# Optimization experiments

Measured on AMD Instinct MI355X. Metric: run time of the kernel, lower is better.

## Reference

```python
import math
import jax, jax.numpy as jnp
import numpy as np

HEADS = 16
REL_WINDOW = 128


def setup_inputs() -> dict:
    key = jax.random.key(0)
    k1, k2, k3, k4, k5 = jax.random.split(key, 5)
    b, s, d = 2, 2048, 1024
    hd = d // HEADS          # 64
    R = 2 * REL_WINDOW + 1   # 257
    return {
        "x": jax.random.normal(k1, (b, s, d), dtype=jnp.float32),
        "Wqkv": jax.random.normal(k2, (3 * d, d), dtype=jnp.float32) * (1.0 / math.sqrt(d)),
        "bqkv": jax.random.normal(k3, (3 * d,), dtype=jnp.float32) * 0.02,
        "Wr": jax.random.normal(k4, (R, hd), dtype=jnp.float32) * (1.0 / math.sqrt(hd)),
        "br": jax.random.normal(k5, (R,), dtype=jnp.float32) * 0.02,
    }


def reference(x, Wqkv, bqkv, Wr, br):
    b, s, d = x.shape
    h = HEADS
    hd = d // h
    w = REL_WINDOW
    scale = math.sqrt(d / h)

    # qkv projection; torch view(b,s,h,3*hd) then chunk(3, dim=-1)
    qkv = (x @ Wqkv.T + bqkv).reshape(b, s, h, 3 * hd)
    q, k, v = jnp.split(qkv, 3, axis=-1)          # each [b,s,h,hd]
    q = q.transpose(0, 2, 1, 3)                   # [b,h,s,hd]
    k = k.transpose(0, 2, 1, 3)
    v = v.transpose(0, 2, 1, 3)

    # content scores
    content = jnp.einsum('bhik,bhjk->bhij', q, k) / scale  # [b,h,s,s]

    # relative position scores: project queries to R logits, gather per (i,j) offset
    idx = jnp.arange(s)
    offsets = jnp.clip(idx[None, :] - idx[:, None], -w, w) + w  # [s,s] in [0, 2w]
    rp = jnp.einsum('bhik,rk->bhir', q, Wr) + br               # [b,h,s,R]
    pos = jnp.take_along_axis(rp, jnp.broadcast_to(offsets, (b, h, s, s)), axis=-1)

    attn = jax.nn.softmax(content + pos, axis=-1)
    out = jnp.einsum('bhij,bhjk->bhik', attn, v)  # [b,h,s,hd]
    return out.transpose(0, 2, 1, 3).reshape(b, s, d)
```

## Files before the change

### kernel.cpp

```cpp
#include <hip/hip_runtime.h>

typedef short bfrag __attribute__((ext_vector_type(8)));
typedef float f32x4 __attribute__((ext_vector_type(4)));

#define MFMA16(a, b, c) __builtin_amdgcn_mfma_f32_16x16x32_bf16((a), (b), (c), 0, 0, 0)

#define SEQ   2048
#define DMOD  1024
#define NHEAD 16
#define HDIM  64
#define RSZ   257
#define RSTRIDE 260
#define RPADN 272
#define XN    (4096*1024)
#define WN    (3072*1024)
#define LOG2E 1.44269504f

__device__ __forceinline__ unsigned short f2bf(float f) {
  unsigned int u = __float_as_uint(f);
  u += 0x7FFFu + ((u >> 16) & 1u);
  return (unsigned short)(u >> 16);
}
__device__ __forceinline__ float bf2f(unsigned short u) {
  return __uint_as_float(((unsigned int)u) << 16);
}
__device__ __forceinline__ unsigned int pkbf(float a, float b) {
#if defined(__gfx950__)
  unsigned int r;
  asm("v_cvt_pk_bf16_f32 %0, %1, %2" : "=v"(r) : "v"(a), "v"(b));
  return r;
#else
  return (unsigned int)f2bf(a) | ((unsigned int)f2bf(b) << 16);
#endif
}
__device__ __forceinline__ float fexp2(float x) {
#if __has_builtin(__builtin_amdgcn_exp2f)
  return __builtin_amdgcn_exp2f(x);
#else
  return __expf(x * 0.69314718f);
#endif
}
__device__ __forceinline__ void gl2lds16(const void* g, void* l) {
  __builtin_amdgcn_global_load_lds(
      (__attribute__((address_space(1))) void*)(g),
      (__attribute__((address_space(3))) void*)(l), 16, 0, 0);
}

__global__ __launch_bounds__(256) void cast_all(const float* __restrict__ x,
                                                const float* __restrict__ Wqkv,
                                                const float* __restrict__ Wr,
                                                unsigned short* __restrict__ xb,
                                                unsigned short* __restrict__ wb,
                                                unsigned short* __restrict__ wrb) {
  int i = (blockIdx.x * 256 + threadIdx.x) * 4;
  if (i < XN) {
    float4 v = *(const float4*)(x + i);
    ushort4 o; o.x = f2bf(v.x); o.y = f2bf(v.y); o.z = f2bf(v.z); o.w = f2bf(v.w);
    *(ushort4*)(xb + i) = o;
  } else if (i < XN + WN) {
    int j = i - XN;
    float4 v = *(const float4*)(Wqkv + j);
    ushort4 o; o.x = f2bf(v.x); o.y = f2bf(v.y); o.z = f2bf(v.z); o.w = f2bf(v.w);
    *(ushort4*)(wb + j) = o;
  } else {
    int j = i - XN - WN;
    ushort4 o;
    unsigned short t[4];
#pragma unroll
    for (int k = 0; k < 4; ++k)
      t[k] = (j + k < RSZ * HDIM) ? f2bf(Wr[j + k]) : (unsigned short)0;
    o.x = t[0]; o.y = t[1]; o.z = t[2]; o.w = t[3];
    *(ushort4*)(wrb + j) = o;
  }
}

__global__ __launch_bounds__(256) void qkv_gemm(const unsigned short* __restrict__ xb,
                                                const unsigned short* __restrict__ wb,
                                                const float* __restrict__ bqkv,
                                                unsigned short* __restrict__ qb,
                                                unsigned short* __restrict__ kbuf,
                                                unsigned short* __restrict__ vtb) {
  __shared__ unsigned short SMEM[2 * 128 * 64];
  unsigned short* As = SMEM;
  unsigned short* Bs = SMEM + 128 * 64;
  unsigned short* Vtmp = SMEM;
  const int tid = threadIdx.x;
  const int m0 = blockIdx.y * 128, n0 = blockIdx.x * 128;
  const int wave = tid >> 6, lane = tid & 63;
  const int q4 = lane >> 4, l16 = lane & 15;
  const int wm = (wave & 1) * 64, wn = (wave >> 1) * 64;
  const int sw = l16 & 7;

  f32x4 acc[4][4];
#pragma unroll
  for (int rt = 0; rt < 4; ++rt)
#pragma unroll
    for (int ct = 0; ct < 4; ++ct) acc[rt][ct] = (f32x4){0.f, 0.f, 0.f, 0.f};

  for (int k0 = 0; k0 < DMOD; k0 += 64) {
#pragma unroll
    for (int it = 0; it < 4; ++it) {
      int ch = it * 256 + tid;
      int r = ch >> 3, cl = (ch & 7) ^ (r & 7);
      gl2lds16(xb + (size_t)(m0 + r) * DMOD + k0 + cl * 8, As + ch * 8);
      gl2lds16(wb + (size_t)(n0 + r) * DMOD + k0 + cl * 8, Bs + ch * 8);
    }
    __syncthreads();
#pragma unroll
    for (int ks = 0; ks < 2; ++ks) {
      bfrag af[4], bf[4];
#pragma unroll
      for (int rt = 0; rt < 4; ++rt)
        af[rt] = *(const bfrag*)(As + (wm + rt * 16 + l16) * 64 + ((ks * 4 + q4) ^ sw) * 8);
#pragma unroll
      for (int ct = 0; ct < 4; ++ct)
        bf[ct] = *(const bfrag*)(Bs + (wn + ct * 16 + l16) * 64 + ((ks * 4 + q4) ^ sw) * 8);
#pragma unroll
      for (int rt = 0; rt < 4; ++rt)
#pragma unroll
        for (int ct = 0; ct < 4; ++ct)
          acc[rt][ct] = MFMA16(bf[ct], af[rt], acc[rt][ct]);
    }
    __syncthreads();
  }

  const int batch = m0 >> 11;
  const int sbase = m0 & 2047;
  const int r3 = blockIdx.x % 3;
  const bool hasV = (r3 != 0);
  const int nv0 = n0 + ((r3 == 2) ? 64 : 0);

#pragma unroll
  for (int ct = 0; ct < 4; ++ct) {
    int ng = n0 + wn + ct * 16 + q4 * 4;
    int hh = ng / 192;
    int rem = ng - hh * 192;
    int t = rem >> 6, dd = rem & 63;
    float4 b4 = *(const float4*)(bqkv + ng);
    if (t < 2) {
      unsigned short* dst = (t == 0) ? qb : kbuf;
      size_t rowo = ((size_t)(batch * NHEAD + hh)) * SEQ + sbase;
#pragma unroll
      for (int rt = 0; rt < 4; ++rt) {
        int m = wm + rt * 16 + l16;
        uint2 pv;
        pv.x = pkbf(acc[rt][ct][0] + b4.x, acc[rt][ct][1] + b4.y);
        pv.y = pkbf(acc[rt][ct][2] + b4.z, acc[rt][ct][3] + b4.w);
        *(uint2*)(dst + (rowo + m) * HDIM + dd) = pv;
      }
    } else {
#pragma unroll
      for (int rt = 0; rt < 4; ++rt) {
        int m = wm + rt * 16 + l16;
        Vtmp[(dd + 0) * 136 + m] = f2bf(acc[rt][ct][0] + b4.x);
        Vtmp[(dd + 1) * 136 + m] = f2bf(acc[rt][ct][1] + b4.y);
        Vtmp[(dd + 2) * 136 + m] = f2bf(acc[rt][ct][2] + b4.z);
        Vtmp[(dd + 3) * 136 + m] = f2bf(acc[rt][ct][3] + b4.w);
      }
    }
  }

  if (hasV) {
    __syncthreads();
    const int hh = nv0 / 192;
    unsigned short* vdst = vtb + ((size_t)(batch * NHEAD + hh)) * HDIM * SEQ;
#pragma unroll
    for (int it = 0; it < 4; ++it) {
      int u = it * 256 + tid;
      int dd = u >> 4, mc = u & 15;
      bfrag val = *(const bfrag*)(Vtmp + dd * 136 + mc * 8);
      *(bfrag*)(vdst + (size_t)dd * SEQ + sbase + mc * 8) = val;
    }
  }
}

__global__ __launch_bounds__(256) void rp_gemm(const unsigned short* __restrict__ qb,
                                               const unsigned short* __restrict__ wrb,
                                               const float* __restrict__ br,
                                               unsigned short* __restrict__ rp16) {
  __shared__ unsigned short WrS[RPADN * HDIM];
  __shared__ unsigned short Qs[64 * HDIM];
  const int tid = threadIdx.x;
  const size_t row0 = (size_t)blockIdx.x * 64;

  for (int i = tid; i < RPADN * HDIM / 8; i += 256)
    *(uint4*)(&WrS[i * 8]) = *(const uint4*)(&wrb[i * 8]);
  for (int i = tid; i < 512; i += 256)
    *(uint4*)(&Qs[i * 8]) = *(const uint4*)(&qb[row0 * HDIM + i * 8]);
  __syncthreads();

  const int wave = tid >> 6, lane = tid & 63;
  const int q4 = lane >> 4, l16 = lane & 15;

  bfrag af0 = *(const bfrag*)(Qs + (wave * 16 + l16) * 64 + q4 * 8);
  bfrag af1 = *(const bfrag*)(Qs + (wave * 16 + l16) * 64 + 32 + q4 * 8);

  unsigned short* rrow = rp16 + (row0 + wave * 16 + l16) * RSTRIDE;
  const float br256 = br[256];

#pragma unroll 4
  for (int ct = 0; ct < 16; ++ct) {
    f32x4 acc = (f32x4){0.f, 0.f, 0.f, 0.f};
    bfrag w0 = *(const bfrag*)(WrS + (ct * 16 + l16) * 64 + q4 * 8);
    bfrag w1 = *(const bfrag*)(WrS + (ct * 16 + l16) * 64 + 32 + q4 * 8);
    acc = MFMA16(w0, af0, acc);
    acc = MFMA16(w1, af1, acc);
    int r = ct * 16 + q4 * 4;
    float4 b4 = *(const float4*)(br + r);
    uint2 pv;
    pv.x = pkbf((acc[0] + b4.x) * LOG2E, (acc[1] + b4.y) * LOG2E);
    pv.y = pkbf((acc[2] + b4.z) * LOG2E, (acc[3] + b4.w) * LOG2E);
    *(uint2*)(rrow + r) = pv;
  }
  {
    f32x4 acc = (f32x4){0.f, 0.f, 0.f, 0.f};
    bfrag w0 = *(const bfrag*)(WrS + (256 + l16) * 64 + q4 * 8);
    bfrag w1 = *(const bfrag*)(WrS + (256 + l16) * 64 + 32 + q4 * 8);
    acc = MFMA16(w0, af0, acc);
    acc = MFMA16(w1, af1, acc);
    if (q4 == 0)
      rrow[256] = f2bf((acc[0] + br256) * LOG2E);
  }
}

__global__ __launch_bounds__(512) void flash_attn(const unsigned short* __restrict__ qb,
                                                  const unsigned short* __restrict__ kbuf,
                                                  const unsigned short* __restrict__ vtb,
                                                  const unsigned short* __restrict__ rp16,
                                                  float* __restrict__ out) {
  __shared__ unsigned short Ks[2][64 * 64];
  __shared__ unsigned short Vs[2][64 * 64];
  __shared__ unsigned short Ps[128 * 64];

  const int tid = threadIdx.x;
  const int orig = blockIdx.x;
  const int slot = orig >> 3;
  const int bh = (orig & 7) * 4 + (slot >> 4);
  const int i0 = (slot & 15) << 7;
  const int wave = tid >> 6, lane = tid & 63;
  const int q4 = lane >> 4, l16 = lane & 15;
  const int sw = l16 & 7;
  const float SC = 0.125f * LOG2E;

  const int rloc = wave * 16 + l16;
  const int ig = i0 + rloc;
  const int iw0 = i0 + wave * 16;
  const unsigned short* qrow = qb + ((size_t)bh * SEQ + ig) * HDIM;
  bfrag qf0 = *(const bfrag*)(qrow + q4 * 8);
  bfrag qf1 = *(const bfrag*)(qrow + 32 + q4 * 8);

  const unsigned short* rpbase = rp16 + ((size_t)bh * SEQ + ig) * RSTRIDE;
  const float rpL = bf2f(rpbase[0]);
  const float rpR = bf2f(rpbase[256]);

  float m_s = -3.0e38f, l_s = 0.f;
  f32x4 oacc[4];
#pragma unroll
  for (int ct = 0; ct < 4; ++ct) oacc[ct] = (f32x4){0.f, 0.f, 0.f, 0.f};

  const unsigned short* kbase = kbuf + (size_t)bh * SEQ * HDIM;
  const unsigned short* vbase = vtb + (size_t)bh * HDIM * SEQ;

  const int sr = tid >> 3, scl = (tid & 7) ^ ((tid >> 3) & 7);

  gl2lds16(kbase + (size_t)sr * HDIM + scl * 8, &Ks[0][tid * 8]);
  gl2lds16(vbase + (size_t)sr * SEQ + 0 + scl * 8, &Vs[0][tid * 8]);
  __syncthreads();

  for (int jt = 0; jt < 32; ++jt) {
    const int cur = jt & 1;
    const int j0 = jt * 64;

    if (jt < 31) {
      gl2lds16(kbase + (size_t)(j0 + 64 + sr) * HDIM + scl * 8, &Ks[cur ^ 1][tid * 8]);
      gl2lds16(vbase + (size_t)sr * SEQ + (j0 + 64) + scl * 8, &Vs[cur ^ 1][tid * 8]);
    }

    f32x4 sacc[4];
#pragma unroll
    for (int ct = 0; ct < 4; ++ct) {
      sacc[ct] = (f32x4){0.f, 0.f, 0.f, 0.f};
      bfrag k0f = *(const bfrag*)(&Ks[cur][(ct * 16 + l16) * 64 + (q4 ^ sw) * 8]);
      bfrag k1f = *(const bfrag*)(&Ks[cur][(ct * 16 + l16) * 64 + ((4 + q4) ^ sw) * 8]);
      sacc[ct] = MFMA16(k0f, qf0, sacc[ct]);
      sacc[ct] = MFMA16(k1f, qf1, sacc[ct]);
    }

    float p[4][4];
    const int djw = j0 - iw0;
    if (djw >= 143) {
#pragma unroll
      for (int ct = 0; ct < 4; ++ct)
#pragma unroll
        for (int reg = 0; reg < 4; ++reg)
          p[ct][reg] = sacc[ct][reg] * SC + rpR;
    } else if (djw <= -191) {
#pragma unroll
      for (int ct = 0; ct < 4; ++ct)
#pragma unroll
        for (int reg = 0; reg < 4; ++reg)
          p[ct][reg] = sacc[ct][reg] * SC + rpL;
    } else {
#pragma unroll
      for (int ct = 0; ct < 4; ++ct) {
#pragma unroll
        for (int reg = 0; reg < 4; ++reg) {
          int j = j0 + ct * 16 + q4 * 4 + reg;
          int off = j - ig;
          off = (off < -128) ? -128 : (off > 128 ? 128 : off);
          p[ct][reg] = sacc[ct][reg] * SC + bf2f(rpbase[off + 128]);
        }
      }
    }

    float mm;
    {
      float a0 = fmaxf(fmaxf(p[0][0], p[0][1]), fmaxf(p[0][2], p[0][3]));
      float a1 = fmaxf(fmaxf(p[1][0], p[1][1]), fmaxf(p[1][2], p[1][3]));
      float a2 = fmaxf(fmaxf(p[2][0], p[2][1]), fmaxf(p[2][2], p[2][3]));
      float a3 = fmaxf(fmaxf(p[3][0], p[3][1]), fmaxf(p[3][2], p[3][3]));
      mm = fmaxf(fmaxf(a0, a1), fmaxf(a2, a3));
      mm = fmaxf(mm, __shfl_xor(mm, 16));
      mm = fmaxf(mm, __shfl_xor(mm, 32));
    }
    if (!__all(mm <= m_s + 8.0f)) {
      const float mnew = fmaxf(m_s, mm);
      const float alpha = fexp2(m_s - mnew);
      m_s = mnew;
      l_s *= alpha;
#pragma unroll
      for (int ct = 0; ct < 4; ++ct)
#pragma unroll
        for (int reg = 0; reg < 4; ++reg)
          oacc[ct][reg] *= alpha;
    }
#pragma unroll
    for (int ct = 0; ct < 4; ++ct)
#pragma unroll
      for (int reg = 0; reg < 4; ++reg)
        p[ct][reg] = fexp2(p[ct][reg] - m_s);
    {
      float s0 = (p[0][0] + p[0][1]) + (p[0][2] + p[0][3]);
      float s1 = (p[1][0] + p[1][1]) + (p[1][2] + p[1][3]);
      float s2 = (p[2][0] + p[2][1]) + (p[2][2] + p[2][3]);
      float s3 = (p[3][0] + p[3][1]) + (p[3][2] + p[3][3]);
      float rs = (s0 + s1) + (s2 + s3);
      rs += __shfl_xor(rs, 16);
      rs += __shfl_xor(rs, 32);
      l_s += rs;
    }

    unsigned int* Pw = (unsigned int*)Ps;
#pragma unroll
    for (int ct = 0; ct < 4; ++ct) {
      unsigned int pk01 = pkbf(p[ct][0], p[ct][1]);
      unsigned int pk23 = pkbf(p[ct][2], p[ct][3]);
      int chunk = ct * 2 + (q4 >> 1);
      unsigned int a = rloc * 32 + ((chunk ^ sw) << 2) + ((q4 & 1) << 1);
      Pw[a] = pk01;
      Pw[a + 1] = pk23;
    }

    bfrag pf0 = *(const bfrag*)(Ps + rloc * 64 + (q4 ^ sw) * 8);
    bfrag pf1 = *(const bfrag*)(Ps + rloc * 64 + ((4 + q4) ^ sw) * 8);
#pragma unroll
    for (int ct = 0; ct < 4; ++ct) {
      bfrag v0f = *(const bfrag*)(&Vs[cur][(ct * 16 + l16) * 64 + (q4 ^ sw) * 8]);
      bfrag v1f = *(const bfrag*)(&Vs[cur][(ct * 16 + l16) * 64 + ((4 + q4) ^ sw) * 8]);
      oacc[ct] = MFMA16(v0f, pf0, oacc[ct]);
      oacc[ct] = MFMA16(v1f, pf1, oacc[ct]);
    }

    __syncthreads();
  }

  const int bidx = bh >> 4, hh = bh & 15;
  const float inv = 1.0f / l_s;
  float* orow = out + ((size_t)bidx * SEQ + ig) * DMOD + hh * HDIM;
#pragma unroll
  for (int ct = 0; ct < 4; ++ct) {
    float4 v;
    v.x = oacc[ct][0] * inv;
    v.y = oacc[ct][1] * inv;
    v.z = oacc[ct][2] * inv;
    v.w = oacc[ct][3] * inv;
    *(float4*)(orow + ct * 16 + q4 * 4) = v;
  }
}

extern "C" void kernel_launch(void* const* d_in, const int* in_sizes, int n_in,
                              void* d_out, int out_size, void* d_ws, size_t ws_size,
                              hipStream_t stream) {
  const float* x    = (const float*)d_in[0];
  const float* Wqkv = (const float*)d_in[1];
  const float* bqkv = (const float*)d_in[2];
  const float* Wr   = (const float*)d_in[3];
  const float* br   = (const float*)d_in[4];
  float* out = (float*)d_out;

  char* ws = (char*)d_ws;
  unsigned short* xb   = (unsigned short*)(ws);
  unsigned short* wb   = (unsigned short*)(ws + 8388608);
  unsigned short* qb   = (unsigned short*)(ws + 14680064);
  unsigned short* kb   = (unsigned short*)(ws + 23068672);
  unsigned short* vtb  = (unsigned short*)(ws + 31457280);
  unsigned short* wrb  = (unsigned short*)(ws + 39845888);
  unsigned short* rp16 = (unsigned short*)(ws + 39880704);

  cast_all<<<7185, 256, 0, stream>>>(x, Wqkv, Wr, xb, wb, wrb);
  qkv_gemm<<<dim3(24, 32), 256, 0, stream>>>(xb, wb, bqkv, qb, kb, vtb);
  rp_gemm<<<1024, 256, 0, stream>>>(qb, wrb, br, rp16);
  flash_attn<<<512, 512, 0, stream>>>(qb, kb, vtb, rp16, out);
}
```

Before: 215.5 us.

## Fuse relative-position projection GEMM into flash attention kernel prologue

Removes the separate rp_gemm launch and computes each query row's 257 relative-position logits inside flash_attn, reusing the query fragments already held in registers. Wr is staged into an LDS region that is later reused for the K/V double buffers, so the kernel's shared-memory footprint stays about the same. The logits are still written to global memory and read back by the same rows, which is why an explicit vmcnt wait and a barrier were added. The aim is to save a kernel launch and the Q reload, at the cost of a longer prologue and an extra sync in the attention kernel.

```diff
diff --git a/kernel.cpp b/kernel.cpp
--- a/kernel.cpp
+++ b/kernel.cpp
@@ -174,63 +174,16 @@
   }
 }
 
-__global__ __launch_bounds__(256) void rp_gemm(const unsigned short* __restrict__ qb,
-                                               const unsigned short* __restrict__ wrb,
-                                               const float* __restrict__ br,
-                                               unsigned short* __restrict__ rp16) {
-  __shared__ unsigned short WrS[RPADN * HDIM];
-  __shared__ unsigned short Qs[64 * HDIM];
-  const int tid = threadIdx.x;
-  const size_t row0 = (size_t)blockIdx.x * 64;
-
-  for (int i = tid; i < RPADN * HDIM / 8; i += 256)
-    *(uint4*)(&WrS[i * 8]) = *(const uint4*)(&wrb[i * 8]);
-  for (int i = tid; i < 512; i += 256)
-    *(uint4*)(&Qs[i * 8]) = *(const uint4*)(&qb[row0 * HDIM + i * 8]);
-  __syncthreads();
-
-  const int wave = tid >> 6, lane = tid & 63;
-  const int q4 = lane >> 4, l16 = lane & 15;
-
-  bfrag af0 = *(const bfrag*)(Qs + (wave * 16 + l16) * 64 + q4 * 8);
-  bfrag af1 = *(const bfrag*)(Qs + (wave * 16 + l16) * 64 + 32 + q4 * 8);
-
-  unsigned short* rrow = rp16 + (row0 + wave * 16 + l16) * RSTRIDE;
-  const float br256 = br[256];
-
-#pragma unroll 4
-  for (int ct = 0; ct < 16; ++ct) {
-    f32x4 acc = (f32x4){0.f, 0.f, 0.f, 0.f};
-    bfrag w0 = *(const bfrag*)(WrS + (ct * 16 + l16) * 64 + q4 * 8);
-    bfrag w1 = *(const bfrag*)(WrS + (ct * 16 + l16) * 64 + 32 + q4 * 8);
-    acc = MFMA16(w0, af0, acc);
-    acc = MFMA16(w1, af1, acc);
-    int r = ct * 16 + q4 * 4;
-    float4 b4 = *(const float4*)(br + r);
-    uint2 pv;
-    pv.x = pkbf((acc[0] + b4.x) * LOG2E, (acc[1] + b4.y) * LOG2E);
-    pv.y = pkbf((acc[2] + b4.z) * LOG2E, (acc[3] + b4.w) * LOG2E);
-    *(uint2*)(rrow + r) = pv;
-  }
-  {
-    f32x4 acc = (f32x4){0.f, 0.f, 0.f, 0.f};
-    bfrag w0 = *(const bfrag*)(WrS + (256 + l16) * 64 + q4 * 8);
-    bfrag w1 = *(const bfrag*)(WrS + (256 + l16) * 64 + 32 + q4 * 8);
-    acc = MFMA16(w0, af0, acc);
-    acc = MFMA16(w1, af1, acc);
-    if (q4 == 0)
-      rrow[256] = f2bf((acc[0] + br256) * LOG2E);
-  }
-}
-
 __global__ __launch_bounds__(512) void flash_attn(const unsigned short* __restrict__ qb,
                                                   const unsigned short* __restrict__ kbuf,
                                                   const unsigned short* __restrict__ vtb,
-                                                  const unsigned short* __restrict__ rp16,
+                                                  const unsigned short* __restrict__ wrb,
+                                                  const float* __restrict__ br,
+                                                  unsigned short* __restrict__ rp16,
                                                   float* __restrict__ out) {
-  __shared__ unsigned short Ks[2][64 * 64];
-  __shared__ unsigned short Vs[2][64 * 64];
-  __shared__ unsigned short Ps[128 * 64];
+  __shared__ unsigned short SMEM[24576];
+  unsigned short* WrS = SMEM;
+  unsigned short* Ps  = SMEM + 16384;
 
   const int tid = threadIdx.x;
   const int orig = blockIdx.x;
@@ -249,7 +202,41 @@
   bfrag qf0 = *(const bfrag*)(qrow + q4 * 8);
   bfrag qf1 = *(const bfrag*)(qrow + 32 + q4 * 8);
 
-  const unsigned short* rpbase = rp16 + ((size_t)bh * SEQ + ig) * RSTRIDE;
+  unsigned short* rpbase = rp16 + ((size_t)bh * SEQ + ig) * RSTRIDE;
+
+  {
+    for (int i = tid; i < RPADN * HDIM / 8; i += 512)
+      *(uint4*)(&WrS[i * 8]) = *(const uint4*)(&wrb[i * 8]);
+    __syncthreads();
+
+    const float br256 = br[256];
+#pragma unroll 4
+    for (int ct = 0; ct < 16; ++ct) {
+      f32x4 acc = (f32x4){0.f, 0.f, 0.f, 0.f};
+      bfrag w0 = *(const bfrag*)(WrS + (ct * 16 + l16) * 64 + q4 * 8);
+      bfrag w1 = *(const bfrag*)(WrS + (ct * 16 + l16) * 64 + 32 + q4 * 8);
+      acc = MFMA16(w0, qf0, acc);
+      acc = MFMA16(w1, qf1, acc);
+      int r = ct * 16 + q4 * 4;
+      float4 b4 = *(const float4*)(br + r);
+      uint2 pv;
+      pv.x = pkbf((acc[0] + b4.x) * LOG2E, (acc[1] + b4.y) * LOG2E);
+      pv.y = pkbf((acc[2] + b4.z) * LOG2E, (acc[3] + b4.w) * LOG2E);
+      *(uint2*)(rpbase + r) = pv;
+    }
+    {
+      f32x4 acc = (f32x4){0.f, 0.f, 0.f, 0.f};
+      bfrag w0 = *(const bfrag*)(WrS + (256 + l16) * 64 + q4 * 8);
+      bfrag w1 = *(const bfrag*)(WrS + (256 + l16) * 64 + 32 + q4 * 8);
+      acc = MFMA16(w0, qf0, acc);
+      acc = MFMA16(w1, qf1, acc);
+      if (q4 == 0)
+        rpbase[256] = f2bf((acc[0] + br256) * LOG2E);
+    }
+    asm volatile("s_waitcnt vmcnt(0)" ::: "memory");
+    __syncthreads();
+  }
+
   const float rpL = bf2f(rpbase[0]);
   const float rpR = bf2f(rpbase[256]);
 
@@ -263,25 +250,29 @@
 
   const int sr = tid >> 3, scl = (tid & 7) ^ ((tid >> 3) & 7);
 
-  gl2lds16(kbase + (size_t)sr * HDIM + scl * 8, &Ks[0][tid * 8]);
-  gl2lds16(vbase + (size_t)sr * SEQ + 0 + scl * 8, &Vs[0][tid * 8]);
+  gl2lds16(kbase + (size_t)sr * HDIM + scl * 8, SMEM + tid * 8);
+  gl2lds16(vbase + (size_t)sr * SEQ + 0 + scl * 8, SMEM + 8192 + tid * 8);
   __syncthreads();
 
   for (int jt = 0; jt < 32; ++jt) {
     const int cur = jt & 1;
     const int j0 = jt * 64;
+    unsigned short* Kc = SMEM + cur * 4096;
+    unsigned short* Vc = SMEM + 8192 + cur * 4096;
 
     if (jt < 31) {
-      gl2lds16(kbase + (size_t)(j0 + 64 + sr) * HDIM + scl * 8, &Ks[cur ^ 1][tid * 8]);
-      gl2lds16(vbase + (size_t)sr * SEQ + (j0 + 64) + scl * 8, &Vs[cur ^ 1][tid * 8]);
+      gl2lds16(kbase + (size_t)(j0 + 64 + sr) * HDIM + scl * 8,
+               SMEM + (cur ^ 1) * 4096 + tid * 8);
+      gl2lds16(vbase + (size_t)sr * SEQ + (j0 + 64) + scl * 8,
+               SMEM + 8192 + (cur ^ 1) * 4096 + tid * 8);
     }
 
     f32x4 sacc[4];
 #pragma unroll
     for (int ct = 0; ct < 4; ++ct) {
       sacc[ct] = (f32x4){0.f, 0.f, 0.f, 0.f};
-      bfrag k0f = *(const bfrag*)(&Ks[cur][(ct * 16 + l16) * 64 + (q4 ^ sw) * 8]);
-      bfrag k1f = *(const bfrag*)(&Ks[cur][(ct * 16 + l16) * 64 + ((4 + q4) ^ sw) * 8]);
+      bfrag k0f = *(const bfrag*)(Kc + (ct * 16 + l16) * 64 + (q4 ^ sw) * 8);
+      bfrag k1f = *(const bfrag*)(Kc + (ct * 16 + l16) * 64 + ((4 + q4) ^ sw) * 8);
       sacc[ct] = MFMA16(k0f, qf0, sacc[ct]);
       sacc[ct] = MFMA16(k1f, qf1, sacc[ct]);
     }
@@ -365,8 +356,8 @@
     bfrag pf1 = *(const bfrag*)(Ps + rloc * 64 + ((4 + q4) ^ sw) * 8);
 #pragma unroll
     for (int ct = 0; ct < 4; ++ct) {
-      bfrag v0f = *(const bfrag*)(&Vs[cur][(ct * 16 + l16) * 64 + (q4 ^ sw) * 8]);
-      bfrag v1f = *(const bfrag*)(&Vs[cur][(ct * 16 + l16) * 64 + ((4 + q4) ^ sw) * 8]);
+      bfrag v0f = *(const bfrag*)(Vc + (ct * 16 + l16) * 64 + (q4 ^ sw) * 8);
+      bfrag v1f = *(const bfrag*)(Vc + (ct * 16 + l16) * 64 + ((4 + q4) ^ sw) * 8);
       oacc[ct] = MFMA16(v0f, pf0, oacc[ct]);
       oacc[ct] = MFMA16(v1f, pf1, oacc[ct]);
     }
@@ -409,6 +400,5 @@
 
   cast_all<<<7185, 256, 0, stream>>>(x, Wqkv, Wr, xb, wb, wrb);
   qkv_gemm<<<dim3(24, 32), 256, 0, stream>>>(xb, wb, bqkv, qb, kb, vtb);
-  rp_gemm<<<1024, 256, 0, stream>>>(qb, wrb, br, rp16);
-  flash_attn<<<512, 512, 0, stream>>>(qb, kb, vtb, rp16, out);
-}
+  flash_attn<<<512, 512, 0, stream>>>(qb, kb, vtb, wrb, br, rp16, out);
+}
```

After: 207.1 us. -3.9%, faster.
